# Performance work log

Hardware: AMD Instinct MI355X
Metric: run time of the kernel (lower is better)

Reference implementation:

```python
import jax, jax.numpy as jnp
import numpy as np

B, T, C, H = 2, 2048, 1024, 16
HD = C // H  # 64

def setup_inputs() -> dict:
    key = jax.random.key(0)
    ks = jax.random.split(key, 9)
    s = 0.02
    return {
        "x": jax.random.normal(ks[0], (B, T, C), jnp.float32),
        "Wq": jax.random.normal(ks[1], (C, C), jnp.float32) * s,
        "bq": jax.random.normal(ks[2], (C,), jnp.float32) * s,
        "Wk": jax.random.normal(ks[3], (C, C), jnp.float32) * s,
        "bk": jax.random.normal(ks[4], (C,), jnp.float32) * s,
        "Wv": jax.random.normal(ks[5], (C, C), jnp.float32) * s,
        "bv": jax.random.normal(ks[6], (C,), jnp.float32) * s,
        "Wp": jax.random.normal(ks[7], (C, C), jnp.float32) * s,
        "bp": jax.random.normal(ks[8], (C,), jnp.float32) * s,
    }

def reference(x, Wq, bq, Wk, bk, Wv, bv, Wp, bp):
    Bb, Tt, Cc = x.shape
    hd = Cc // H
    # project and split heads: [B, H, T, hd]
    def heads(W, b):
        return (x @ W.T + b).reshape(Bb, Tt, H, hd).transpose(0, 2, 1, 3)
    q, k, v = heads(Wq, bq), heads(Wk, bk), heads(Wv, bv)
    scale = 1.0 / np.sqrt(hd).astype(np.float32)
    att = jnp.einsum('bhqd,bhkd->bhqk', q, k) * scale
    causal = jnp.tril(jnp.ones((Tt, Tt), bool))
    att = jnp.where(causal[None, None], att, -jnp.inf)
    att = jax.nn.softmax(att, axis=-1)
    y = jnp.einsum('bhqk,bhkd->bhqd', att, v)
    y = y.transpose(0, 2, 1, 3).reshape(Bb, Tt, Cc)
    return y @ Wp.T + bp
```

## Files before the change

kernel.cpp:

```cpp
#include <hip/hip_runtime.h>
#include <hip/hip_bf16.h>

#define Tsz 2048
#define Csz 1024
#define Hn 16

typedef short s8v __attribute__((ext_vector_type(8)));
typedef short s4v __attribute__((ext_vector_type(4)));
typedef float f4v __attribute__((ext_vector_type(4)));

#define QSCALE (0.125f * 1.44269504088896f)

__device__ __forceinline__ unsigned short bfr(float x) {
    return (unsigned short)((__builtin_bit_cast(unsigned, x) + 0x8000u) >> 16);
}
__device__ __forceinline__ unsigned pack2_rn(float a, float b) {
    const unsigned ua = __builtin_bit_cast(unsigned, a) + 0x8000u;
    const unsigned ub = __builtin_bit_cast(unsigned, b) + 0x8000u;
    return (ua >> 16) | (ub & 0xFFFF0000u);
}

__device__ __forceinline__ void gload_lds(const void* g, void* l) {
    __builtin_amdgcn_global_load_lds(
        (const __attribute__((address_space(1))) void*)g,
        (__attribute__((address_space(3))) void*)l, 16, 0, 0);
}

__global__ void cvt6(const float* __restrict__ x, const float* __restrict__ wq,
                     const float* __restrict__ wk, const float* __restrict__ wv,
                     const float* __restrict__ wp,
                     short* __restrict__ xo, short* __restrict__ qo,
                     short* __restrict__ ko, short* __restrict__ vo,
                     short* __restrict__ po) {
    const int bx = blockIdx.x;
    const float* in; short* out; int ib;
    if (bx < 4096) { in = x; out = xo; ib = bx; }
    else {
        const int r = bx - 4096, w = r >> 10;
        ib = r & 1023;
        switch (w) {
            case 0: in = wq; out = qo; break;
            case 1: in = wk; out = ko; break;
            case 2: in = wv; out = vo; break;
            default: in = wp; out = po; break;
        }
    }
    const int i = ib * 1024 + threadIdx.x * 4;
    float4 v = *(const float4*)(in + i);
    int2 o;
    o.x = (int)pack2_rn(v.x, v.y);
    o.y = (int)pack2_rn(v.z, v.w);
    *(int2*)(out + i) = o;
}

__global__ __launch_bounds__(256, 3) void qkv_gemm(
    const short* __restrict__ X,
    const short* __restrict__ Wq, const short* __restrict__ Wk, const short* __restrict__ Wv,
    const float* __restrict__ bq, const float* __restrict__ bk, const float* __restrict__ bv,
    short* __restrict__ Qo, short* __restrict__ Ko, short* __restrict__ Vto)
{
    const int z = blockIdx.z;
    const short* W = (z == 0) ? Wq : (z == 1) ? Wk : Wv;
    const float* bias = (z == 0) ? bq : (z == 1) ? bk : bv;

    __shared__ __align__(16) short Ash[128 * 32];
    __shared__ __align__(16) short Bsh[128 * 32];
    __shared__ __align__(16) short TR[64 * 72];

    const int tid = threadIdx.x, lane = tid & 63, wave = tid >> 6;
    const int ln = lane & 15, hi = lane >> 4;
    const int m0 = blockIdx.x * 128, n0 = blockIdx.y * 128;
    const int wm = (wave >> 1) * 64, wn = (wave & 1) * 64;

    const short* Ag = X + (size_t)(m0 + (tid >> 2)) * Csz + (tid & 3) * 8;
    const short* Bg = W + (size_t)(n0 + (tid >> 2)) * Csz + (tid & 3) * 8;

    f4v acc[4][4];
    #pragma unroll
    for (int mt = 0; mt < 4; mt++)
        #pragma unroll
        for (int nt = 0; nt < 4; nt++)
            #pragma unroll
            for (int i = 0; i < 4; i++) acc[mt][nt][i] = 0.f;

    for (int k0 = 0; k0 < Csz; k0 += 32) {
        __syncthreads();
        gload_lds(Ag + k0, Ash + tid * 8);
        gload_lds(Ag + k0 + (size_t)64 * Csz, Ash + 2048 + tid * 8);
        gload_lds(Bg + k0, Bsh + tid * 8);
        gload_lds(Bg + k0 + (size_t)64 * Csz, Bsh + 2048 + tid * 8);
        __syncthreads();

        s8v af[4], bfr_[4];
        #pragma unroll
        for (int mt = 0; mt < 4; mt++)
            af[mt] = *(const s8v*)(Ash + (wm + mt * 16 + ln) * 32 + hi * 8);
        #pragma unroll
        for (int nt = 0; nt < 4; nt++)
            bfr_[nt] = *(const s8v*)(Bsh + (wn + nt * 16 + ln) * 32 + hi * 8);
        #pragma unroll
        for (int mt = 0; mt < 4; mt++)
            #pragma unroll
            for (int nt = 0; nt < 4; nt++)
                acc[mt][nt] = __builtin_amdgcn_mfma_f32_16x16x32_bf16(af[mt], bfr_[nt], acc[mt][nt], 0, 0, 0);
    }

    if (z == 2) {
        const int b = m0 >> 11, t0 = m0 & 2047;
        float bvv[4];
        #pragma unroll
        for (int nt = 0; nt < 4; nt++) bvv[nt] = bias[n0 + wn + nt * 16 + ln];
        #pragma unroll
        for (int ph = 0; ph < 4; ph++) {
            const int mh = ph >> 1, nh = ph & 1;
            __syncthreads();
            if ((wave >> 1) == mh && (wave & 1) == nh) {
                #pragma unroll
                for (int mt = 0; mt < 4; mt++)
                    #pragma unroll
                    for (int nt = 0; nt < 4; nt++) {
                        int2 pk;
                        pk.x = (int)pack2_rn(acc[mt][nt][0] + bvv[nt], acc[mt][nt][1] + bvv[nt]);
                        pk.y = (int)pack2_rn(acc[mt][nt][2] + bvv[nt], acc[mt][nt][3] + bvv[nt]);
                        *(int2*)(TR + (nt * 16 + ln) * 72 + mt * 16 + hi * 4) = pk;
                    }
            }
            __syncthreads();
            const int chl = tid >> 2, seg = tid & 3;
            const s8v r0 = *(const s8v*)(TR + chl * 72 + seg * 16);
            const s8v r1 = *(const s8v*)(TR + chl * 72 + seg * 16 + 8);
            short* dst = Vto + (size_t)(b * 1024 + n0 + nh * 64 + chl) * Tsz + t0 + mh * 64 + seg * 16;
            *(s8v*)(dst) = r0;
            *(s8v*)(dst + 8) = r1;
        }
        return;
    }

    const float scale = (z == 0) ? QSCALE : 1.0f;
    short* out = (z == 0) ? Qo : Ko;

    #pragma unroll
    for (int nt = 0; nt < 4; nt++) {
        const int col = n0 + wn + nt * 16 + ln;
        const float bvv = bias[col];
        #pragma unroll
        for (int mt = 0; mt < 4; mt++) {
            const int row0 = m0 + wm + mt * 16 + hi * 4;
            #pragma unroll
            for (int i = 0; i < 4; i++)
                out[(size_t)(row0 + i) * Csz + col] = (short)bfr((acc[mt][nt][i] + bvv) * scale);
        }
    }
}

__global__ __launch_bounds__(256, 2) void proj_gemm(
    const short* __restrict__ A, const short* __restrict__ W,
    const float* __restrict__ bias, float* __restrict__ out)
{
    __shared__ __align__(16) short Ash[128 * 32];
    __shared__ __align__(16) short Bsh[64 * 32];

    const int tid = threadIdx.x, lane = tid & 63, wave = tid >> 6;
    const int ln = lane & 15, hi = lane >> 4;
    const int m0 = blockIdx.x * 128, n0 = blockIdx.y * 64;
    const int wm = (wave >> 1) * 64, wn = (wave & 1) * 32;

    const short* Ag = A + (size_t)(m0 + (tid >> 2)) * Csz + (tid & 3) * 8;
    const short* Bg = W + (size_t)(n0 + (tid >> 2)) * Csz + (tid & 3) * 8;

    f4v acc[4][2];
    #pragma unroll
    for (int mt = 0; mt < 4; mt++)
        #pragma unroll
        for (int nt = 0; nt < 2; nt++)
            #pragma unroll
            for (int i = 0; i < 4; i++) acc[mt][nt][i] = 0.f;

    for (int k0 = 0; k0 < Csz; k0 += 32) {
        __syncthreads();
        gload_lds(Ag + k0, Ash + tid * 8);
        gload_lds(Ag + k0 + (size_t)64 * Csz, Ash + 2048 + tid * 8);
        gload_lds(Bg + k0, Bsh + tid * 8);
        __syncthreads();

        s8v af[4], bfr_[2];
        #pragma unroll
        for (int mt = 0; mt < 4; mt++)
            af[mt] = *(const s8v*)(Ash + (wm + mt * 16 + ln) * 32 + hi * 8);
        #pragma unroll
        for (int nt = 0; nt < 2; nt++)
            bfr_[nt] = *(const s8v*)(Bsh + (wn + nt * 16 + ln) * 32 + hi * 8);
        #pragma unroll
        for (int mt = 0; mt < 4; mt++)
            #pragma unroll
            for (int nt = 0; nt < 2; nt++)
                acc[mt][nt] = __builtin_amdgcn_mfma_f32_16x16x32_bf16(af[mt], bfr_[nt], acc[mt][nt], 0, 0, 0);
    }

    #pragma unroll
    for (int nt = 0; nt < 2; nt++) {
        const int col = n0 + wn + nt * 16 + ln;
        const float bvv = bias[col];
        #pragma unroll
        for (int mt = 0; mt < 4; mt++)
            #pragma unroll
            for (int i = 0; i < 4; i++)
                out[(size_t)(m0 + wm + mt * 16 + hi * 4 + i) * Csz + col] = acc[mt][nt][i] + bvv;
    }
}

__global__ __launch_bounds__(512, 2) void attn9(
    const short* __restrict__ Q, const short* __restrict__ Kg,
    const short* __restrict__ Vt, short* __restrict__ Y)
{
    __shared__ __align__(16) short Ksh[2][64 * 72];
    __shared__ __align__(16) short Vsh[2][64 * 72];
    __shared__ __align__(16) short Psh[8][16 * 72];

    const int tid = threadIdx.x, lane = tid & 63, wave = tid >> 6;
    const int wv = wave & 3, g = wave >> 2;
    const int ln = lane & 15, hi = lane >> 4;
    const int p = blockIdx.x;
    const int qts[2] = { g ? 15 - p : p, g ? 16 + p : 31 - p };
    const int bh = blockIdx.y;
    const size_t base = (size_t)(bh >> 4) * Tsz * Csz + (size_t)(bh & 15) * 64;
    const size_t vtbase = (size_t)bh * 64 * Tsz;
    const int qrel = wv * 16 + ln;
    short* Pq = Psh[wave];

    s8v qf[2][2];
    #pragma unroll
    for (int t = 0; t < 2; t++)
        #pragma unroll
        for (int kk = 0; kk < 2; kk++)
            qf[t][kk] = *(const s8v*)(Q + base + (size_t)(qts[t] * 64 + qrel) * Csz + kk * 32 + hi * 8);

    f4v o[2][4];
    float lsum[2] = {0.f, 0.f};
    #pragma unroll
    for (int t = 0; t < 2; t++)
        #pragma unroll
        for (int dt = 0; dt < 4; dt++)
            #pragma unroll
            for (int i = 0; i < 4; i++) o[t][dt][i] = 0.f;

    const int sr = tid >> 3, sc = (tid & 7) * 8;
    const short* Kp = Kg + base + (size_t)sr * Csz + sc;
    const short* Vp = Vt + vtbase + (size_t)sr * Tsz + sc;
    const int swo = sr * 72 + sc;

    const int nkb = 32 - p;

    s8v kR = *(const s8v*)(Kp);
    s8v vR = *(const s8v*)(Vp);
    *(s8v*)(&Ksh[0][swo]) = kR;
    *(s8v*)(&Vsh[0][swo]) = vR;
    kR = *(const s8v*)(Kp + (size_t)64 * Csz);
    vR = *(const s8v*)(Vp + 64);
    __syncthreads();

    for (int kb = 0; kb < nkb; kb++) {
        const int buf = kb & 1;
        if (kb + 1 < nkb) {
            *(s8v*)(&Ksh[buf ^ 1][swo]) = kR;
            *(s8v*)(&Vsh[buf ^ 1][swo]) = vR;
            const int knx = (kb + 2 < nkb) ? (kb + 2) * 64 : (nkb - 1) * 64;
            kR = *(const s8v*)(Kp + (size_t)knx * Csz);
            vR = *(const s8v*)(Vp + knx);
        }

        s8v kf[2][4], vf[2][4];
        #pragma unroll
        for (int nt = 0; nt < 4; nt++)
            #pragma unroll
            for (int kk = 0; kk < 2; kk++) {
                kf[kk][nt] = *(const s8v*)(&Ksh[buf][(nt * 16 + ln) * 72 + kk * 32 + hi * 8]);
                vf[kk][nt] = *(const s8v*)(&Vsh[buf][(nt * 16 + ln) * 72 + kk * 32 + hi * 8]);
            }

        #pragma unroll
        for (int t = 0; t < 2; t++) {
            if (kb > qts[t]) continue;
            const bool dg = (kb == qts[t]);

            f4v s[4];
            #pragma unroll
            for (int nt = 0; nt < 4; nt++) {
                #pragma unroll
                for (int i = 0; i < 4; i++) s[nt][i] = 0.f;
                s[nt] = __builtin_amdgcn_mfma_f32_16x16x32_bf16(kf[0][nt], qf[t][0], s[nt], 0, 0, 0);
                s[nt] = __builtin_amdgcn_mfma_f32_16x16x32_bf16(kf[1][nt], qf[t][1], s[nt], 0, 0, 0);
            }

            #pragma unroll
            for (int nt = 0; nt < 4; nt++) {
                float pv[4];
                #pragma unroll
                for (int i = 0; i < 4; i++) pv[i] = exp2f(s[nt][i]);
                if (dg) {
                    const int kr = nt * 16 + hi * 4;
                    #pragma unroll
                    for (int i = 0; i < 4; i++)
                        if (kr + i > qrel) pv[i] = 0.f;
                }
                lsum[t] += (pv[0] + pv[1]) + (pv[2] + pv[3]);
                int2 w;
                w.x = (int)pack2_rn(pv[0], pv[1]);
                w.y = (int)pack2_rn(pv[2], pv[3]);
                *(int2*)(Pq + ln * 72 + nt * 16 + hi * 4) = w;
            }
            const s8v pb0 = *(const s8v*)(Pq + ln * 72 + hi * 8);
            const s8v pb1 = *(const s8v*)(Pq + ln * 72 + 32 + hi * 8);

            #pragma unroll
            for (int dt = 0; dt < 4; dt++) {
                o[t][dt] = __builtin_amdgcn_mfma_f32_16x16x32_bf16(vf[0][dt], pb0, o[t][dt], 0, 0, 0);
                o[t][dt] = __builtin_amdgcn_mfma_f32_16x16x32_bf16(vf[1][dt], pb1, o[t][dt], 0, 0, 0);
            }
        }
        __syncthreads();
    }

    #pragma unroll
    for (int t = 0; t < 2; t++) {
        float l = lsum[t];
        l += __shfl_xor(l, 16);
        l += __shfl_xor(l, 32);
        const float inv = 1.0f / l;
        const int qrow = qts[t] * 64 + qrel;
        #pragma unroll
        for (int dt = 0; dt < 4; dt++) {
            int2 w;
            w.x = (int)pack2_rn(o[t][dt][0] * inv, o[t][dt][1] * inv);
            w.y = (int)pack2_rn(o[t][dt][2] * inv, o[t][dt][3] * inv);
            *(int2*)(Y + base + (size_t)qrow * Csz + dt * 16 + hi * 4) = w;
        }
    }
}

extern "C" void kernel_launch(void* const* d_in, const int* in_sizes, int n_in,
                              void* d_out, int out_size, void* d_ws, size_t ws_size,
                              hipStream_t stream) {
    const float* x  = (const float*)d_in[0];
    const float* Wq = (const float*)d_in[1];
    const float* bq = (const float*)d_in[2];
    const float* Wk = (const float*)d_in[3];
    const float* bk = (const float*)d_in[4];
    const float* Wv = (const float*)d_in[5];
    const float* bv = (const float*)d_in[6];
    const float* Wp = (const float*)d_in[7];
    const float* bp = (const float*)d_in[8];

    char* ws = (char*)d_ws;
    short* Xb  = (short*)(ws);
    short* Wqb = (short*)(ws + (8u  << 20));
    short* Wkb = (short*)(ws + (10u << 20));
    short* Wvb = (short*)(ws + (12u << 20));
    short* Wpb = (short*)(ws + (14u << 20));
    short* Qb  = (short*)(ws + (16u << 20));
    short* Kb  = (short*)(ws + (24u << 20));
    short* Vtb = (short*)(ws + (32u << 20));
    short* Yb  = (short*)(ws + (40u << 20));

    hipLaunchKernelGGL(cvt6, dim3(8192), dim3(256), 0, stream,
                       x, Wq, Wk, Wv, Wp, Xb, Wqb, Wkb, Wvb, Wpb);

    hipLaunchKernelGGL(qkv_gemm, dim3(32, 8, 3), dim3(256), 0, stream,
                       Xb, Wqb, Wkb, Wvb, bq, bk, bv, Qb, Kb, Vtb);

    hipLaunchKernelGGL(attn9, dim3(8, 32), dim3(512), 0, stream, Qb, Kb, Vtb, Yb);

    hipLaunchKernelGGL(proj_gemm, dim3(32, 16), dim3(256), 0, stream, Yb, Wpb, bp, (float*)d_out);
}
```

Baseline: 189.1 us.

## Merge all four kernels into one cooperative persistent kernel with grid syncs

Replaces the four separate launches (conversion, QKV GEMM, attention, projection) with a single cooperative kernel of 256 blocks of 512 threads that separates the phases with grid.sync. The QKV GEMM is restructured so each block computes Q, K and V for one 128x128 tile, sharing the X tile loads across the three weights. Launch gaps and kernel boundaries are removed. In exchange, every phase is fixed to 256 blocks: the GEMMs lose the extra occupancy of the earlier larger grids, grid barriers add latency, and the QKV tile keeps three accumulator sets live, which raises register pressure.

```diff
diff --git a/kernel.cpp b/kernel.cpp
--- a/kernel.cpp
+++ b/kernel.cpp
@@ -1,9 +1,11 @@
 #include <hip/hip_runtime.h>
 #include <hip/hip_bf16.h>
+#include <hip/hip_cooperative_groups.h>
+
+namespace cg = cooperative_groups;
 
 #define Tsz 2048
 #define Csz 1024
-#define Hn 16
 
 typedef short s8v __attribute__((ext_vector_type(8)));
 typedef short s4v __attribute__((ext_vector_type(4)));
@@ -26,314 +28,312 @@
         (__attribute__((address_space(3))) void*)l, 16, 0, 0);
 }
 
-__global__ void cvt6(const float* __restrict__ x, const float* __restrict__ wq,
-                     const float* __restrict__ wk, const float* __restrict__ wv,
-                     const float* __restrict__ wp,
-                     short* __restrict__ xo, short* __restrict__ qo,
-                     short* __restrict__ ko, short* __restrict__ vo,
-                     short* __restrict__ po) {
-    const int bx = blockIdx.x;
-    const float* in; short* out; int ib;
-    if (bx < 4096) { in = x; out = xo; ib = bx; }
-    else {
-        const int r = bx - 4096, w = r >> 10;
-        ib = r & 1023;
-        switch (w) {
-            case 0: in = wq; out = qo; break;
-            case 1: in = wk; out = ko; break;
-            case 2: in = wv; out = vo; break;
-            default: in = wp; out = po; break;
-        }
-    }
-    const int i = ib * 1024 + threadIdx.x * 4;
-    float4 v = *(const float4*)(in + i);
-    int2 o;
-    o.x = (int)pack2_rn(v.x, v.y);
-    o.y = (int)pack2_rn(v.z, v.w);
-    *(int2*)(out + i) = o;
-}
-
-__global__ __launch_bounds__(256, 3) void qkv_gemm(
-    const short* __restrict__ X,
-    const short* __restrict__ Wq, const short* __restrict__ Wk, const short* __restrict__ Wv,
-    const float* __restrict__ bq, const float* __restrict__ bk, const float* __restrict__ bv,
-    short* __restrict__ Qo, short* __restrict__ Ko, short* __restrict__ Vto)
+__device__ __forceinline__ void cvt_range(const float* __restrict__ in,
+                                          short* __restrict__ out,
+                                          int n4, int gtid, int gstride) {
+    for (int i = gtid; i < n4; i += gstride) {
+        float4 v = ((const float4*)in)[i];
+        int2 o;
+        o.x = (int)pack2_rn(v.x, v.y);
+        o.y = (int)pack2_rn(v.z, v.w);
+        ((int2*)out)[i] = o;
+    }
+}
+
+__global__ __launch_bounds__(512, 2) void mega(
+    const float* __restrict__ x,
+    const float* __restrict__ Wq, const float* __restrict__ bq,
+    const float* __restrict__ Wk, const float* __restrict__ bk,
+    const float* __restrict__ Wv, const float* __restrict__ bv,
+    const float* __restrict__ Wp, const float* __restrict__ bp,
+    float* __restrict__ out,
+    short* __restrict__ Xb, short* __restrict__ Wqb, short* __restrict__ Wkb,
+    short* __restrict__ Wvb, short* __restrict__ Wpb,
+    short* __restrict__ Qb, short* __restrict__ Kb, short* __restrict__ Vtb,
+    short* __restrict__ Yb)
 {
-    const int z = blockIdx.z;
-    const short* W = (z == 0) ? Wq : (z == 1) ? Wk : Wv;
-    const float* bias = (z == 0) ? bq : (z == 1) ? bk : bv;
-
-    __shared__ __align__(16) short Ash[128 * 32];
-    __shared__ __align__(16) short Bsh[128 * 32];
-    __shared__ __align__(16) short TR[64 * 72];
+    __shared__ __align__(16) short smem[27648];
+    cg::grid_group grid = cg::this_grid();
 
     const int tid = threadIdx.x, lane = tid & 63, wave = tid >> 6;
     const int ln = lane & 15, hi = lane >> 4;
-    const int m0 = blockIdx.x * 128, n0 = blockIdx.y * 128;
-    const int wm = (wave >> 1) * 64, wn = (wave & 1) * 64;
-
-    const short* Ag = X + (size_t)(m0 + (tid >> 2)) * Csz + (tid & 3) * 8;
-    const short* Bg = W + (size_t)(n0 + (tid >> 2)) * Csz + (tid & 3) * 8;
-
-    f4v acc[4][4];
-    #pragma unroll
-    for (int mt = 0; mt < 4; mt++)
-        #pragma unroll
-        for (int nt = 0; nt < 4; nt++)
-            #pragma unroll
-            for (int i = 0; i < 4; i++) acc[mt][nt][i] = 0.f;
-
-    for (int k0 = 0; k0 < Csz; k0 += 32) {
+    const int blk = blockIdx.x;
+
+    {
+        const int gtid = blk * 512 + tid, gs = 256 * 512;
+        cvt_range(x,  Xb,  1048576, gtid, gs);
+        cvt_range(Wq, Wqb, 262144, gtid, gs);
+        cvt_range(Wk, Wkb, 262144, gtid, gs);
+        cvt_range(Wv, Wvb, 262144, gtid, gs);
+        cvt_range(Wp, Wpb, 262144, gtid, gs);
+    }
+    __threadfence();
+    grid.sync();
+
+    {
+        short* Ash = smem;
+        short* Bq_ = smem + 4096;
+        short* Bk_ = smem + 8192;
+        short* Bv_ = smem + 12288;
+        const int m0 = (blk >> 3) * 128, n0 = (blk & 7) * 128;
+        const int wm = (wave >> 2) * 64, wn = (wave & 3) * 32;
+
+        const short* Ag = Xb  + (size_t)(m0 + (tid >> 2)) * Csz + (tid & 3) * 8;
+        const short* Qg = Wqb + (size_t)(n0 + (tid >> 2)) * Csz + (tid & 3) * 8;
+        const short* Kgp = Wkb + (size_t)(n0 + (tid >> 2)) * Csz + (tid & 3) * 8;
+        const short* Vg = Wvb + (size_t)(n0 + (tid >> 2)) * Csz + (tid & 3) * 8;
+
+        f4v aq[4][2], ak[4][2], av[4][2];
+        #pragma unroll
+        for (int mt = 0; mt < 4; mt++)
+            #pragma unroll
+            for (int nt = 0; nt < 2; nt++)
+                #pragma unroll
+                for (int i = 0; i < 4; i++) { aq[mt][nt][i] = 0.f; ak[mt][nt][i] = 0.f; av[mt][nt][i] = 0.f; }
+
+        for (int k0 = 0; k0 < Csz; k0 += 32) {
+            __syncthreads();
+            gload_lds(Ag + k0, Ash + tid * 8);
+            gload_lds(Qg + k0, Bq_ + tid * 8);
+            gload_lds(Kgp + k0, Bk_ + tid * 8);
+            gload_lds(Vg + k0, Bv_ + tid * 8);
+            __syncthreads();
+
+            s8v af[4];
+            #pragma unroll
+            for (int mt = 0; mt < 4; mt++)
+                af[mt] = *(const s8v*)(Ash + (wm + mt * 16 + ln) * 32 + hi * 8);
+            #pragma unroll
+            for (int nt = 0; nt < 2; nt++) {
+                const int ro = (wn + nt * 16 + ln) * 32 + hi * 8;
+                const s8v fq = *(const s8v*)(Bq_ + ro);
+                const s8v fk = *(const s8v*)(Bk_ + ro);
+                const s8v fv = *(const s8v*)(Bv_ + ro);
+                #pragma unroll
+                for (int mt = 0; mt < 4; mt++) {
+                    aq[mt][nt] = __builtin_amdgcn_mfma_f32_16x16x32_bf16(af[mt], fq, aq[mt][nt], 0, 0, 0);
+                    ak[mt][nt] = __builtin_amdgcn_mfma_f32_16x16x32_bf16(af[mt], fk, ak[mt][nt], 0, 0, 0);
+                    av[mt][nt] = __builtin_amdgcn_mfma_f32_16x16x32_bf16(af[mt], fv, av[mt][nt], 0, 0, 0);
+                }
+            }
+        }
+
+        #pragma unroll
+        for (int nt = 0; nt < 2; nt++) {
+            const int col = n0 + wn + nt * 16 + ln;
+            const float bqv = bq[col], bkv = bk[col];
+            #pragma unroll
+            for (int mt = 0; mt < 4; mt++) {
+                const int row0 = m0 + wm + mt * 16 + hi * 4;
+                #pragma unroll
+                for (int i = 0; i < 4; i++) {
+                    Qb[(size_t)(row0 + i) * Csz + col] = (short)bfr((aq[mt][nt][i] + bqv) * QSCALE);
+                    Kb[(size_t)(row0 + i) * Csz + col] = (short)bfr(ak[mt][nt][i] + bkv);
+                }
+            }
+        }
+        {
+            short* TR = smem + 16384;
+            float bvv[2];
+            #pragma unroll
+            for (int nt = 0; nt < 2; nt++) bvv[nt] = bv[n0 + wn + nt * 16 + ln];
+            const int b_ = m0 >> 11, t0 = m0 & 2047;
+            #pragma unroll
+            for (int ph = 0; ph < 4; ph++) {
+                const int mh = ph >> 1, nh = ph & 1;
+                __syncthreads();
+                if ((wave >> 2) == mh && ((wave >> 1) & 1) == nh) {
+                    #pragma unroll
+                    for (int mt = 0; mt < 4; mt++)
+                        #pragma unroll
+                        for (int nt = 0; nt < 2; nt++) {
+                            int2 pk;
+                            pk.x = (int)pack2_rn(av[mt][nt][0] + bvv[nt], av[mt][nt][1] + bvv[nt]);
+                            pk.y = (int)pack2_rn(av[mt][nt][2] + bvv[nt], av[mt][nt][3] + bvv[nt]);
+                            *(int2*)(TR + ((wave & 1) * 32 + nt * 16 + ln) * 72 + mt * 16 + hi * 4) = pk;
+                        }
+                }
+                __syncthreads();
+                const int chl = tid >> 3, seg = tid & 7;
+                const s8v r = *(const s8v*)(TR + chl * 72 + seg * 8);
+                *(s8v*)(Vtb + (size_t)(b_ * 1024 + n0 + nh * 64 + chl) * Tsz + t0 + mh * 64 + seg * 8) = r;
+            }
+        }
+    }
+    __threadfence();
+    grid.sync();
+
+    {
+        short* Ksh = smem;
+        short* Vsh = smem + 9216;
+        short* Pq  = smem + 18432 + wave * 1152;
+
+        const int wv = wave & 3, g = wave >> 2;
+        const int p = blk & 7;
+        const int bh = blk >> 3;
+        const int qts[2] = { g ? 15 - p : p, g ? 16 + p : 31 - p };
+        const size_t base = (size_t)(bh >> 4) * Tsz * Csz + (size_t)(bh & 15) * 64;
+        const size_t vtbase = (size_t)bh * 64 * Tsz;
+        const int qrel = wv * 16 + ln;
+
+        s8v qf[2][2];
+        #pragma unroll
+        for (int t = 0; t < 2; t++)
+            #pragma unroll
+            for (int kk = 0; kk < 2; kk++)
+                qf[t][kk] = *(const s8v*)(Qb + base + (size_t)(qts[t] * 64 + qrel) * Csz + kk * 32 + hi * 8);
+
+        f4v o[2][4];
+        float lsum[2] = {0.f, 0.f};
+        #pragma unroll
+        for (int t = 0; t < 2; t++)
+            #pragma unroll
+            for (int dt = 0; dt < 4; dt++)
+                #pragma unroll
+                for (int i = 0; i < 4; i++) o[t][dt][i] = 0.f;
+
+        const int sr = tid >> 3, sc = (tid & 7) * 8;
+        const short* Kp = Kb + base + (size_t)sr * Csz + sc;
+        const short* Vp = Vtb + vtbase + (size_t)sr * Tsz + sc;
+        const int swo = sr * 72 + sc;
+
+        const int nkb = 32 - p;
+
+        s8v kR = *(const s8v*)(Kp);
+        s8v vR = *(const s8v*)(Vp);
+        *(s8v*)(Ksh + swo) = kR;
+        *(s8v*)(Vsh + swo) = vR;
+        kR = *(const s8v*)(Kp + (size_t)64 * Csz);
+        vR = *(const s8v*)(Vp + 64);
         __syncthreads();
-        gload_lds(Ag + k0, Ash + tid * 8);
-        gload_lds(Ag + k0 + (size_t)64 * Csz, Ash + 2048 + tid * 8);
-        gload_lds(Bg + k0, Bsh + tid * 8);
-        gload_lds(Bg + k0 + (size_t)64 * Csz, Bsh + 2048 + tid * 8);
-        __syncthreads();
-
-        s8v af[4], bfr_[4];
+
+        for (int kb = 0; kb < nkb; kb++) {
+            const int buf = kb & 1;
+            if (kb + 1 < nkb) {
+                *(s8v*)(Ksh + (buf ^ 1) * 4608 + swo) = kR;
+                *(s8v*)(Vsh + (buf ^ 1) * 4608 + swo) = vR;
+                const int knx = (kb + 2 < nkb) ? (kb + 2) * 64 : (nkb - 1) * 64;
+                kR = *(const s8v*)(Kp + (size_t)knx * Csz);
+                vR = *(const s8v*)(Vp + knx);
+            }
+
+            s8v kf[2][4], vf[2][4];
+            #pragma unroll
+            for (int nt = 0; nt < 4; nt++)
+                #pragma unroll
+                for (int kk = 0; kk < 2; kk++) {
+                    kf[kk][nt] = *(const s8v*)(Ksh + buf * 4608 + (nt * 16 + ln) * 72 + kk * 32 + hi * 8);
+                    vf[kk][nt] = *(const s8v*)(Vsh + buf * 4608 + (nt * 16 + ln) * 72 + kk * 32 + hi * 8);
+                }
+
+            #pragma unroll
+            for (int t = 0; t < 2; t++) {
+                if (kb > qts[t]) continue;
+                const bool dg = (kb == qts[t]);
+
+                f4v s[4];
+                #pragma unroll
+                for (int nt = 0; nt < 4; nt++) {
+                    #pragma unroll
+                    for (int i = 0; i < 4; i++) s[nt][i] = 0.f;
+                    s[nt] = __builtin_amdgcn_mfma_f32_16x16x32_bf16(kf[0][nt], qf[t][0], s[nt], 0, 0, 0);
+                    s[nt] = __builtin_amdgcn_mfma_f32_16x16x32_bf16(kf[1][nt], qf[t][1], s[nt], 0, 0, 0);
+                }
+
+                #pragma unroll
+                for (int nt = 0; nt < 4; nt++) {
+                    float pv[4];
+                    #pragma unroll
+                    for (int i = 0; i < 4; i++) pv[i] = exp2f(s[nt][i]);
+                    if (dg) {
+                        const int kr = nt * 16 + hi * 4;
+                        #pragma unroll
+                        for (int i = 0; i < 4; i++)
+                            if (kr + i > qrel) pv[i] = 0.f;
+                    }
+                    lsum[t] += (pv[0] + pv[1]) + (pv[2] + pv[3]);
+                    int2 w;
+                    w.x = (int)pack2_rn(pv[0], pv[1]);
+                    w.y = (int)pack2_rn(pv[2], pv[3]);
+                    *(int2*)(Pq + ln * 72 + nt * 16 + hi * 4) = w;
+                }
+                const s8v pb0 = *(const s8v*)(Pq + ln * 72 + hi * 8);
+                const s8v pb1 = *(const s8v*)(Pq + ln * 72 + 32 + hi * 8);
+
+                #pragma unroll
+                for (int dt = 0; dt < 4; dt++) {
+                    o[t][dt] = __builtin_amdgcn_mfma_f32_16x16x32_bf16(vf[0][dt], pb0, o[t][dt], 0, 0, 0);
+                    o[t][dt] = __builtin_amdgcn_mfma_f32_16x16x32_bf16(vf[1][dt], pb1, o[t][dt], 0, 0, 0);
+                }
+            }
+            __syncthreads();
+        }
+
+        #pragma unroll
+        for (int t = 0; t < 2; t++) {
+            float l = lsum[t];
+            l += __shfl_xor(l, 16);
+            l += __shfl_xor(l, 32);
+            const float inv = 1.0f / l;
+            const int qrow = qts[t] * 64 + qrel;
+            #pragma unroll
+            for (int dt = 0; dt < 4; dt++) {
+                int2 w;
+                w.x = (int)pack2_rn(o[t][dt][0] * inv, o[t][dt][1] * inv);
+                w.y = (int)pack2_rn(o[t][dt][2] * inv, o[t][dt][3] * inv);
+                *(int2*)(Yb + base + (size_t)qrow * Csz + dt * 16 + hi * 4) = w;
+            }
+        }
+    }
+    __threadfence();
+    grid.sync();
+
+    {
+        short* Ash = smem;
+        short* Bsh = smem + 4096;
+        const int m0 = (blk >> 3) * 128, n0 = (blk & 7) * 128;
+        const int wm = (wave >> 2) * 64, wn = (wave & 3) * 32;
+
+        const short* Ag = Yb  + (size_t)(m0 + (tid >> 2)) * Csz + (tid & 3) * 8;
+        const short* Bg = Wpb + (size_t)(n0 + (tid >> 2)) * Csz + (tid & 3) * 8;
+
+        f4v acc[4][2];
         #pragma unroll
         for (int mt = 0; mt < 4; mt++)
-            af[mt] = *(const s8v*)(Ash + (wm + mt * 16 + ln) * 32 + hi * 8);
-        #pragma unroll
-        for (int nt = 0; nt < 4; nt++)
-            bfr_[nt] = *(const s8v*)(Bsh + (wn + nt * 16 + ln) * 32 + hi * 8);
-        #pragma unroll
-        for (int mt = 0; mt < 4; mt++)
-            #pragma unroll
-            for (int nt = 0; nt < 4; nt++)
-                acc[mt][nt] = __builtin_amdgcn_mfma_f32_16x16x32_bf16(af[mt], bfr_[nt], acc[mt][nt], 0, 0, 0);
-    }
-
-    if (z == 2) {
-        const int b = m0 >> 11, t0 = m0 & 2047;
-        float bvv[4];
-        #pragma unroll
-        for (int nt = 0; nt < 4; nt++) bvv[nt] = bias[n0 + wn + nt * 16 + ln];
-        #pragma unroll
-        for (int ph = 0; ph < 4; ph++) {
-            const int mh = ph >> 1, nh = ph & 1;
-            __syncthreads();
-            if ((wave >> 1) == mh && (wave & 1) == nh) {
-                #pragma unroll
-                for (int mt = 0; mt < 4; mt++)
-                    #pragma unroll
-                    for (int nt = 0; nt < 4; nt++) {
-                        int2 pk;
-                        pk.x = (int)pack2_rn(acc[mt][nt][0] + bvv[nt], acc[mt][nt][1] + bvv[nt]);
-                        pk.y = (int)pack2_rn(acc[mt][nt][2] + bvv[nt], acc[mt][nt][3] + bvv[nt]);
-                        *(int2*)(TR + (nt * 16 + ln) * 72 + mt * 16 + hi * 4) = pk;
-                    }
-            }
-            __syncthreads();
-            const int chl = tid >> 2, seg = tid & 3;
-            const s8v r0 = *(const s8v*)(TR + chl * 72 + seg * 16);
-            const s8v r1 = *(const s8v*)(TR + chl * 72 + seg * 16 + 8);
-            short* dst = Vto + (size_t)(b * 1024 + n0 + nh * 64 + chl) * Tsz + t0 + mh * 64 + seg * 16;
-            *(s8v*)(dst) = r0;
-            *(s8v*)(dst + 8) = r1;
-        }
-        return;
-    }
-
-    const float scale = (z == 0) ? QSCALE : 1.0f;
-    short* out = (z == 0) ? Qo : Ko;
-
-    #pragma unroll
-    for (int nt = 0; nt < 4; nt++) {
-        const int col = n0 + wn + nt * 16 + ln;
-        const float bvv = bias[col];
-        #pragma unroll
-        for (int mt = 0; mt < 4; mt++) {
-            const int row0 = m0 + wm + mt * 16 + hi * 4;
-            #pragma unroll
-            for (int i = 0; i < 4; i++)
-                out[(size_t)(row0 + i) * Csz + col] = (short)bfr((acc[mt][nt][i] + bvv) * scale);
-        }
-    }
-}
-
-__global__ __launch_bounds__(256, 2) void proj_gemm(
-    const short* __restrict__ A, const short* __restrict__ W,
-    const float* __restrict__ bias, float* __restrict__ out)
-{
-    __shared__ __align__(16) short Ash[128 * 32];
-    __shared__ __align__(16) short Bsh[64 * 32];
-
-    const int tid = threadIdx.x, lane = tid & 63, wave = tid >> 6;
-    const int ln = lane & 15, hi = lane >> 4;
-    const int m0 = blockIdx.x * 128, n0 = blockIdx.y * 64;
-    const int wm = (wave >> 1) * 64, wn = (wave & 1) * 32;
-
-    const short* Ag = A + (size_t)(m0 + (tid >> 2)) * Csz + (tid & 3) * 8;
-    const short* Bg = W + (size_t)(n0 + (tid >> 2)) * Csz + (tid & 3) * 8;
-
-    f4v acc[4][2];
-    #pragma unroll
-    for (int mt = 0; mt < 4; mt++)
-        #pragma unroll
-        for (int nt = 0; nt < 2; nt++)
-            #pragma unroll
-            for (int i = 0; i < 4; i++) acc[mt][nt][i] = 0.f;
-
-    for (int k0 = 0; k0 < Csz; k0 += 32) {
-        __syncthreads();
-        gload_lds(Ag + k0, Ash + tid * 8);
-        gload_lds(Ag + k0 + (size_t)64 * Csz, Ash + 2048 + tid * 8);
-        gload_lds(Bg + k0, Bsh + tid * 8);
-        __syncthreads();
-
-        s8v af[4], bfr_[2];
-        #pragma unroll
-        for (int mt = 0; mt < 4; mt++)
-            af[mt] = *(const s8v*)(Ash + (wm + mt * 16 + ln) * 32 + hi * 8);
-        #pragma unroll
-        for (int nt = 0; nt < 2; nt++)
-            bfr_[nt] = *(const s8v*)(Bsh + (wn + nt * 16 + ln) * 32 + hi * 8);
-        #pragma unroll
-        for (int mt = 0; mt < 4; mt++)
             #pragma unroll
             for (int nt = 0; nt < 2; nt++)
-                acc[mt][nt] = __builtin_amdgcn_mfma_f32_16x16x32_bf16(af[mt], bfr_[nt], acc[mt][nt], 0, 0, 0);
-    }
-
-    #pragma unroll
-    for (int nt = 0; nt < 2; nt++) {
-        const int col = n0 + wn + nt * 16 + ln;
-        const float bvv = bias[col];
-        #pragma unroll
-        for (int mt = 0; mt < 4; mt++)
-            #pragma unroll
-            for (int i = 0; i < 4; i++)
-                out[(size_t)(m0 + wm + mt * 16 + hi * 4 + i) * Csz + col] = acc[mt][nt][i] + bvv;
-    }
-}
-
-__global__ __launch_bounds__(512, 2) void attn9(
-    const short* __restrict__ Q, const short* __restrict__ Kg,
-    const short* __restrict__ Vt, short* __restrict__ Y)
-{
-    __shared__ __align__(16) short Ksh[2][64 * 72];
-    __shared__ __align__(16) short Vsh[2][64 * 72];
-    __shared__ __align__(16) short Psh[8][16 * 72];
-
-    const int tid = threadIdx.x, lane = tid & 63, wave = tid >> 6;
-    const int wv = wave & 3, g = wave >> 2;
-    const int ln = lane & 15, hi = lane >> 4;
-    const int p = blockIdx.x;
-    const int qts[2] = { g ? 15 - p : p, g ? 16 + p : 31 - p };
-    const int bh = blockIdx.y;
-    const size_t base = (size_t)(bh >> 4) * Tsz * Csz + (size_t)(bh & 15) * 64;
-    const size_t vtbase = (size_t)bh * 64 * Tsz;
-    const int qrel = wv * 16 + ln;
-    short* Pq = Psh[wave];
-
-    s8v qf[2][2];
-    #pragma unroll
-    for (int t = 0; t < 2; t++)
-        #pragma unroll
-        for (int kk = 0; kk < 2; kk++)
-            qf[t][kk] = *(const s8v*)(Q + base + (size_t)(qts[t] * 64 + qrel) * Csz + kk * 32 + hi * 8);
-
-    f4v o[2][4];
-    float lsum[2] = {0.f, 0.f};
-    #pragma unroll
-    for (int t = 0; t < 2; t++)
-        #pragma unroll
-        for (int dt = 0; dt < 4; dt++)
-            #pragma unroll
-            for (int i = 0; i < 4; i++) o[t][dt][i] = 0.f;
-
-    const int sr = tid >> 3, sc = (tid & 7) * 8;
-    const short* Kp = Kg + base + (size_t)sr * Csz + sc;
-    const short* Vp = Vt + vtbase + (size_t)sr * Tsz + sc;
-    const int swo = sr * 72 + sc;
-
-    const int nkb = 32 - p;
-
-    s8v kR = *(const s8v*)(Kp);
-    s8v vR = *(const s8v*)(Vp);
-    *(s8v*)(&Ksh[0][swo]) = kR;
-    *(s8v*)(&Vsh[0][swo]) = vR;
-    kR = *(const s8v*)(Kp + (size_t)64 * Csz);
-    vR = *(const s8v*)(Vp + 64);
-    __syncthreads();
-
-    for (int kb = 0; kb < nkb; kb++) {
-        const int buf = kb & 1;
-        if (kb + 1 < nkb) {
-            *(s8v*)(&Ksh[buf ^ 1][swo]) = kR;
-            *(s8v*)(&Vsh[buf ^ 1][swo]) = vR;
-            const int knx = (kb + 2 < nkb) ? (kb + 2) * 64 : (nkb - 1) * 64;
-            kR = *(const s8v*)(Kp + (size_t)knx * Csz);
-            vR = *(const s8v*)(Vp + knx);
-        }
-
-        s8v kf[2][4], vf[2][4];
-        #pragma unroll
-        for (int nt = 0; nt < 4; nt++)
-            #pragma unroll
-            for (int kk = 0; kk < 2; kk++) {
-                kf[kk][nt] = *(const s8v*)(&Ksh[buf][(nt * 16 + ln) * 72 + kk * 32 + hi * 8]);
-                vf[kk][nt] = *(const s8v*)(&Vsh[buf][(nt * 16 + ln) * 72 + kk * 32 + hi * 8]);
-            }
-
-        #pragma unroll
-        for (int t = 0; t < 2; t++) {
-            if (kb > qts[t]) continue;
-            const bool dg = (kb == qts[t]);
-
-            f4v s[4];
-            #pragma unroll
-            for (int nt = 0; nt < 4; nt++) {
-                #pragma unroll
-                for (int i = 0; i < 4; i++) s[nt][i] = 0.f;
-                s[nt] = __builtin_amdgcn_mfma_f32_16x16x32_bf16(kf[0][nt], qf[t][0], s[nt], 0, 0, 0);
-                s[nt] = __builtin_amdgcn_mfma_f32_16x16x32_bf16(kf[1][nt], qf[t][1], s[nt], 0, 0, 0);
-            }
-
-            #pragma unroll
-            for (int nt = 0; nt < 4; nt++) {
-                float pv[4];
-                #pragma unroll
-                for (int i = 0; i < 4; i++) pv[i] = exp2f(s[nt][i]);
-                if (dg) {
-                    const int kr = nt * 16 + hi * 4;
-                    #pragma unroll
-                    for (int i = 0; i < 4; i++)
-                        if (kr + i > qrel) pv[i] = 0.f;
-                }
-                lsum[t] += (pv[0] + pv[1]) + (pv[2] + pv[3]);
-                int2 w;
-                w.x = (int)pack2_rn(pv[0], pv[1]);
-                w.y = (int)pack2_rn(pv[2], pv[3]);
-                *(int2*)(Pq + ln * 72 + nt * 16 + hi * 4) = w;
-            }
-            const s8v pb0 = *(const s8v*)(Pq + ln * 72 + hi * 8);
-            const s8v pb1 = *(const s8v*)(Pq + ln * 72 + 32 + hi * 8);
-
-            #pragma unroll
-            for (int dt = 0; dt < 4; dt++) {
-                o[t][dt] = __builtin_amdgcn_mfma_f32_16x16x32_bf16(vf[0][dt], pb0, o[t][dt], 0, 0, 0);
-                o[t][dt] = __builtin_amdgcn_mfma_f32_16x16x32_bf16(vf[1][dt], pb1, o[t][dt], 0, 0, 0);
-            }
-        }
-        __syncthreads();
-    }
-
-    #pragma unroll
-    for (int t = 0; t < 2; t++) {
-        float l = lsum[t];
-        l += __shfl_xor(l, 16);
-        l += __shfl_xor(l, 32);
-        const float inv = 1.0f / l;
-        const int qrow = qts[t] * 64 + qrel;
-        #pragma unroll
-        for (int dt = 0; dt < 4; dt++) {
-            int2 w;
-            w.x = (int)pack2_rn(o[t][dt][0] * inv, o[t][dt][1] * inv);
-            w.y = (int)pack2_rn(o[t][dt][2] * inv, o[t][dt][3] * inv);
-            *(int2*)(Y + base + (size_t)qrow * Csz + dt * 16 + hi * 4) = w;
+                #pragma unroll
+                for (int i = 0; i < 4; i++) acc[mt][nt][i] = 0.f;
+
+        for (int k0 = 0; k0 < Csz; k0 += 32) {
+            __syncthreads();
+            gload_lds(Ag + k0, Ash + tid * 8);
+            gload_lds(Bg + k0, Bsh + tid * 8);
+            __syncthreads();
+
+            s8v af[4], bfr_[2];
+            #pragma unroll
+            for (int mt = 0; mt < 4; mt++)
+                af[mt] = *(const s8v*)(Ash + (wm + mt * 16 + ln) * 32 + hi * 8);
+            #pragma unroll
+            for (int nt = 0; nt < 2; nt++)
+                bfr_[nt] = *(const s8v*)(Bsh + (wn + nt * 16 + ln) * 32 + hi * 8);
+            #pragma unroll
+            for (int mt = 0; mt < 4; mt++)
+                #pragma unroll
+                for (int nt = 0; nt < 2; nt++)
+                    acc[mt][nt] = __builtin_amdgcn_mfma_f32_16x16x32_bf16(af[mt], bfr_[nt], acc[mt][nt], 0, 0, 0);
+        }
+
+        #pragma unroll
+        for (int nt = 0; nt < 2; nt++) {
+            const int col = n0 + wn + nt * 16 + ln;
+            const float bvv = bp[col];
+            #pragma unroll
+            for (int mt = 0; mt < 4; mt++)
+                #pragma unroll
+                for (int i = 0; i < 4; i++)
+                    out[(size_t)(m0 + wm + mt * 16 + hi * 4 + i) * Csz + col] = acc[mt][nt][i] + bvv;
         }
     }
 }
@@ -350,6 +350,7 @@
     const float* bv = (const float*)d_in[6];
     const float* Wp = (const float*)d_in[7];
     const float* bp = (const float*)d_in[8];
+    float* outp = (float*)d_out;
 
     char* ws = (char*)d_ws;
     short* Xb  = (short*)(ws);
@@ -362,13 +363,11 @@
     short* Vtb = (short*)(ws + (32u << 20));
     short* Yb  = (short*)(ws + (40u << 20));
 
-    hipLaunchKernelGGL(cvt6, dim3(8192), dim3(256), 0, stream,
-                       x, Wq, Wk, Wv, Wp, Xb, Wqb, Wkb, Wvb, Wpb);
-
-    hipLaunchKernelGGL(qkv_gemm, dim3(32, 8, 3), dim3(256), 0, stream,
-                       Xb, Wqb, Wkb, Wvb, bq, bk, bv, Qb, Kb, Vtb);
-
-    hipLaunchKernelGGL(attn9, dim3(8, 32), dim3(512), 0, stream, Qb, Kb, Vtb, Yb);
-
-    hipLaunchKernelGGL(proj_gemm, dim3(32, 16), dim3(256), 0, stream, Yb, Wpb, bp, (float*)d_out);
-}
+    void* kargs[] = {
+        (void*)&x, (void*)&Wq, (void*)&bq, (void*)&Wk, (void*)&bk,
+        (void*)&Wv, (void*)&bv, (void*)&Wp, (void*)&bp, (void*)&outp,
+        (void*)&Xb, (void*)&Wqb, (void*)&Wkb, (void*)&Wvb, (void*)&Wpb,
+        (void*)&Qb, (void*)&Kb, (void*)&Vtb, (void*)&Yb
+    };
+    hipLaunchCooperativeKernel((const void*)mega, dim3(256), dim3(512), kargs, 0, stream);
+}
```

Measured after the change: 442.4 us. +133.9%, slower.
